# Optimization experiments

Hardware: AMD Instinct MI355X
Metric: run time of the kernel (lower is better)

Reference implementation:

```python
import jax, jax.numpy as jnp
import numpy as np

NB, NA, NDF = 4, 512, 3
N = NB * NA
E_FIX = 40960
RADIUS = 3.1
BOX = 13.9  # box side -> ~20 neighbors within radius 3.1
SQRT3 = float(np.sqrt(3.0))
INV_SQRT2 = float(1.0 / np.sqrt(2.0))
INV_SQRT3 = float(1.0 / np.sqrt(3.0))
INV_SQRT6 = float(1.0 / np.sqrt(6.0))
# e3nn FullyConnectedTensorProduct path weights: sqrt(ir_out.dim / sum_fan_in)
PW1_000 = float(np.sqrt(0.5)); PW1_110 = float(np.sqrt(0.5))
PW1_011 = float(np.sqrt(1.5)); PW1_101 = float(np.sqrt(1.5))
PW1_111 = float(np.sqrt(3.0)); PW1_112 = float(np.sqrt(5.0))
PW2 = float(np.sqrt(3.0 / 128.0))  # fan_in = 64+24+24+16

def _w3j_112():
    # real Wigner-3j (1,1,2), unit Frobenius norm (unique up to sign)
    C = np.zeros((3, 3, 5))
    C[0, 1, 0] = C[1, 0, 0] = 1.0                      # xy
    C[1, 2, 1] = C[2, 1, 1] = 1.0                      # yz
    s = 1.0 / np.sqrt(3.0)
    C[2, 2, 2] = 2 * s; C[0, 0, 2] = -s; C[1, 1, 2] = -s  # 3z^2-r^2
    C[0, 2, 3] = C[2, 0, 3] = 1.0                      # zx
    C[0, 0, 4] = 1.0; C[1, 1, 4] = -1.0                # x^2-y^2
    return (C / np.linalg.norm(C)).astype(np.float32)

C112 = jnp.asarray(_w3j_112())
C211 = jnp.transpose(C112, (2, 0, 1))  # (5,3,3)

def _sh(v):
    # o3.spherical_harmonics(l<=1, normalize=False, 'component'): [1, sqrt(3)*v]
    return jnp.concatenate([jnp.ones(v.shape[:-1] + (1,), v.dtype), SQRT3 * v], axis=-1)

def setup_inputs() -> dict:
    rng = np.random.default_rng(0)
    pos = (rng.random((NB, NA, 3)) * BOX).astype(np.float32)
    srcs, dsts = [], []
    for b in range(NB):  # radius_graph per batch (setup-time, numpy)
        d = np.linalg.norm(pos[b][:, None] - pos[b][None, :], axis=-1)
        m = (d < RADIUS) & ~np.eye(NA, dtype=bool)
        i, j = np.nonzero(m)
        srcs.append(i + b * NA); dsts.append(j + b * NA)
    src = np.concatenate(srcs).astype(np.int64)
    dst = np.concatenate(dsts).astype(np.int64)
    if len(src) >= E_FIX:
        src, dst = src[:E_FIX], dst[:E_FIX]
    else:
        pad = E_FIX - len(src)
        src = np.concatenate([src, np.zeros(pad, np.int64)])
        dst = np.concatenate([dst, np.full(pad, N, np.int64)])  # dummy segment, dropped
    key = jax.random.key(0)
    ks = jax.random.split(key, 12)
    f32 = jnp.float32
    return {
        'node_features': jax.random.randint(ks[0], (NB, NA, NDF), 0, 100),
        'r': jnp.asarray(pos),
        'edge_src': jnp.asarray(src, jnp.int32),
        'edge_dst': jnp.asarray(dst, jnp.int32),
        'emb': jax.random.normal(ks[1], (100, 3), f32),
        't1_000': jax.random.normal(ks[2], (64,), f32),
        't1_011': jax.random.normal(ks[3], (24,), f32),
        't1_101': jax.random.normal(ks[4], (24,), f32),
        't1_110': jax.random.normal(ks[5], (64,), f32),
        't1_111': jax.random.normal(ks[6], (24,), f32),
        't1_112': jax.random.normal(ks[7], (16,), f32),
        't2_0e': jax.random.normal(ks[8], (64,), f32),
        't2_1e': jax.random.normal(ks[9], (24,), f32),
        't2_1o': jax.random.normal(ks[10], (24,), f32),
        't2_2e': jax.random.normal(ks[11], (16,), f32),
    }

def reference(node_features, r, edge_src, edge_dst, emb,
              t1_000, t1_011, t1_101, t1_110, t1_111, t1_112,
              t2_0e, t2_1e, t2_1o, t2_2e):
    nb, na, _ = r.shape
    n = nb * na
    rv = r.reshape(-1, 3)
    evec = rv[edge_src] - rv[edge_dst]
    esh = _sh(evec)                      # [E,4]
    s0, s1 = esh[:, :1], esh[:, 1:]      # [E,1], [E,3]
    nf = node_features.reshape(-1, node_features.shape[-1])
    nfe_sh = _sh(emb[nf])                # [n,NDF,4]

    def seg(x):
        return jax.ops.segment_sum(x, edge_dst, num_segments=n + 1)[:n] * INV_SQRT2

    h = jnp.concatenate([seg(esh)[:, None, :], nfe_sh], axis=1)  # [n,C,4]
    x1 = h[edge_src]                                             # [E,C,4]
    a0, a1 = x1[:, :, 0], x1[:, :, 1:4]
    E_, C_ = a0.shape
    # --- tp1: FullyConnectedTensorProduct(sh, sh -> 64x0e+24x1e+24x1o+16x2e+16x2o)
    o0e = (PW1_000 * (a0 * s0))[..., None] * t1_000 \
        + (PW1_110 * INV_SQRT3) * jnp.einsum('eci,ei->ec', a1, s1)[..., None] * t1_110  # [E,C,64]
    p011 = (PW1_011 * INV_SQRT3) * a0[..., None] * s1[:, None, :]   # [E,C,3]
    p101 = (PW1_101 * INV_SQRT3) * a1 * s0[:, None, :]              # [E,C,3]
    o1o = p011[:, :, None, :] * t1_011[:, None] + p101[:, :, None, :] * t1_101[:, None]  # [E,C,24,3]
    o1e = (PW1_111 * INV_SQRT6) * jnp.cross(a1, s1[:, None, :])[:, :, None, :] * t1_111[:, None]
    o2e = PW1_112 * jnp.einsum('eci,ej,ijk->eck', a1, s1, C112)[:, :, None, :] * t1_112[:, None]
    edge_mid = jnp.concatenate([
        o0e,
        o1o.reshape(E_, C_, 72),
        o1e.reshape(E_, C_, 72),
        o2e.reshape(E_, C_, 80),
        jnp.zeros((E_, C_, 80), x1.dtype),  # 16x2o: no allowed path
    ], axis=-1)                              # [E,C,368]
    h2 = seg(edge_mid)[edge_src]             # [E,C,368]
    # --- tp2: FullyConnectedTensorProduct(mid, sh -> 1x1o)
    m0 = h2[:, :, :64]
    m1e = h2[:, :, 64:136].reshape(E_, C_, 24, 3)
    m1o = h2[:, :, 136:208].reshape(E_, C_, 24, 3)
    m2e = h2[:, :, 208:288].reshape(E_, C_, 16, 5)
    q1 = INV_SQRT3 * jnp.einsum('ecu,ej,u->ecj', m0, s1, t2_0e)
    q2 = INV_SQRT6 * jnp.einsum('ecuk,u->eck', jnp.cross(m1e, s1[:, None, None, :]), t2_1e)
    q3 = INV_SQRT3 * jnp.einsum('ecuj,u->ecj', m1o, t2_1o) * s0[:, None, :]
    q4 = jnp.einsum('ecui,ej,ijk,u->eck', m2e, s1, C211, t2_2e)
    edge_out = PW2 * (q1 + q2 + q3 + q4)     # [E,C,3]
    return seg(edge_out).sum(axis=1).reshape(nb, na, 3)
```

## Files before the change

### kernel.cpp

```cpp
#include <hip/hip_runtime.h>

#define INV_SQRT2 0.70710678118654752f
#define SQRT3     1.73205080756887729f
#define INV_SQRT3 0.57735026918962576f
#define INV_SQRT6 0.40824829046386302f
#define PW1_000   0.70710678118654752f
#define PW1_112   2.23606797749978970f
#define K_P       0.70710678118654752f
#define K_V0      0.40824829046386302f
#define PW2       0.15309310892394863f
#define NC        0.31622776601683794f
#define NC2       0.18257418583505537f

#define RED8(v)  { v += __shfl_xor(v,1,8);  v += __shfl_xor(v,2,8);  v += __shfl_xor(v,4,8); }
#define RED16(v) { v += __shfl_xor(v,1,16); v += __shfl_xor(v,2,16); \
                   v += __shfl_xor(v,4,16); v += __shfl_xor(v,8,16); }

__device__ __forceinline__ int lbound(const int* __restrict__ esrc,
                                      const int* __restrict__ edst,
                                      int n, int E, int target) {
    int lo = 0, hi = E;
    while (lo < hi) {
        int mid = (lo + hi) >> 1;
        int d = edst[mid];
        int key = (d >= n) ? n : esrc[mid];
        if (key < target) lo = mid + 1; else hi = mid;
    }
    return lo;
}

__global__ void __launch_bounds__(256) k_prep(
    const int* __restrict__ nf, const float* __restrict__ rv,
    const int* __restrict__ esrc, const int* __restrict__ edst,
    const float* __restrict__ emb,
    const float* __restrict__ t1_000, const float* __restrict__ t1_011,
    const float* __restrict__ t1_101, const float* __restrict__ t1_110,
    const float* __restrict__ t1_111, const float* __restrict__ t1_112,
    const float* __restrict__ t2_0e, const float* __restrict__ t2_1e,
    const float* __restrict__ t2_1o, const float* __restrict__ t2_2e,
    float* __restrict__ Dd, float4* __restrict__ Hsum,
    int* __restrict__ offs, float4* __restrict__ s1arr,
    int n, int E, int nodeBlocks)
{
    if ((int)blockIdx.x == nodeBlocks) {
        int l = threadIdx.x;
        if (l >= 64) return;
        auto wdot = [&](const float* a, const float* b, int len) -> float {
            float v = (l < len) ? a[l] * b[l] : 0.0f;
            for (int off = 32; off > 0; off >>= 1) v += __shfl_down(v, off);
            return v;
        };
        float d0 = wdot(t1_000, t2_0e, 64);
        float d1 = wdot(t1_110, t2_0e, 64);
        float d2 = wdot(t1_011, t2_1e, 24);
        float d3 = wdot(t1_101, t2_1e, 24);
        float d4 = wdot(t1_111, t2_1o, 24);
        float d5 = wdot(t1_112, t2_2e, 16);
        if (l == 0) { Dd[0]=d0; Dd[1]=d1; Dd[2]=d2; Dd[3]=d3; Dd[4]=d4; Dd[5]=d5; }
        return;
    }
    const int tid = blockIdx.x * 256 + threadIdx.x;
    const int nth = nodeBlocks * 256;

    for (int e = tid; e < E; e += nth) {
        int d = edst[e];
        if (d < n) {
            int s = esrc[e];
            s1arr[e] = make_float4(SQRT3*(rv[d*3+0]-rv[s*3+0]),
                                   SQRT3*(rv[d*3+1]-rv[s*3+1]),
                                   SQRT3*(rv[d*3+2]-rv[s*3+2]),
                                   __int_as_float(d));
        } else {
            s1arr[e] = make_float4(0.f, 0.f, 0.f, __int_as_float(0));
        }
    }

    if (tid < n * 8) {
        int v = tid >> 3, ln = tid & 7;
        int b = 0;
        if (ln == 0) b = lbound(esrc, edst, n, E, v);
        if (ln == 1) b = lbound(esrc, edst, n, E, v + 1);
        int lo = __shfl(b, 0, 8);
        int hi = __shfl(b, 1, 8);
        float sx = 0.f, sy = 0.f, sz = 0.f;
        for (int p = lo + ln; p < hi; p += 8) {
            int j = edst[p];
            sx += rv[j*3+0]; sy += rv[j*3+1]; sz += rv[j*3+2];
        }
        RED8(sx) RED8(sy) RED8(sz)
        if (ln == 0) {
            float cnt = (float)(hi - lo);
            float rx = rv[v*3+0], ry = rv[v*3+1], rz = rv[v*3+2];
            float hx = INV_SQRT2 * SQRT3 * (sx - cnt*rx);
            float hy = INV_SQRT2 * SQRT3 * (sy - cnt*ry);
            float hz = INV_SQRT2 * SQRT3 * (sz - cnt*rz);
            int i0 = nf[v*3+0], i1 = nf[v*3+1], i2 = nf[v*3+2];
            float ex = emb[i0*3+0] + emb[i1*3+0] + emb[i2*3+0];
            float ey = emb[i0*3+1] + emb[i1*3+1] + emb[i2*3+1];
            float ez = emb[i0*3+2] + emb[i1*3+2] + emb[i2*3+2];
            Hsum[v] = make_float4(INV_SQRT2*cnt + 3.0f,
                                  hx + SQRT3*ex, hy + SQRT3*ey, hz + SQRT3*ez);
            offs[v] = lo;
            if (v == n - 1) offs[n] = hi;
        }
    }
}

__global__ void __launch_bounds__(256) k_g2(
    const float4* __restrict__ s1arr, const int* __restrict__ offs,
    const float4* __restrict__ Hsum, float* __restrict__ Mid, int n)
{
    int tid = blockIdx.x * blockDim.x + threadIdx.x;
    if (tid >= n * 16) return;
    int v = tid >> 4, ln = tid & 15;
    int lo = offs[v], hi = offs[v+1];
    float A0=0.f, A1=0.f;
    float px=0.f, py=0.f, pz=0.f;
    float qx=0.f, qy=0.f, qz=0.f;
    float cx=0.f, cy=0.f, cz=0.f;
    float t0=0.f, t1=0.f, t2=0.f, t3=0.f, t4=0.f;
    for (int p = lo + ln; p < hi; p += 16) {
        float4 t = s1arr[p];
        int j = __float_as_int(t.w);
        float s1x = t.x, s1y = t.y, s1z = t.z;
        float4 a = Hsum[j];
        float a0 = a.x, a1x = a.y, a1y = a.z, a1z = a.w;
        A0 += a0;
        A1 += a1x*s1x + a1y*s1y + a1z*s1z;
        px += a0*s1x; py += a0*s1y; pz += a0*s1z;
        qx += a1x;    qy += a1y;    qz += a1z;
        cx += a1y*s1z - a1z*s1y;
        cy += a1z*s1x - a1x*s1z;
        cz += a1x*s1y - a1y*s1x;
        t0 += a1x*s1y + a1y*s1x;
        t1 += a1y*s1z + a1z*s1y;
        t2 += 2.0f*a1z*s1z - a1x*s1x - a1y*s1y;
        t3 += a1x*s1z + a1z*s1x;
        t4 += a1x*s1x - a1y*s1y;
    }
    RED16(A0) RED16(A1)
    RED16(px) RED16(py) RED16(pz)
    RED16(qx) RED16(qy) RED16(qz)
    RED16(cx) RED16(cy) RED16(cz)
    RED16(t0) RED16(t1) RED16(t2) RED16(t3) RED16(t4)
    if (ln == 0) {
        const float kA = INV_SQRT2 * PW1_000;
        const float kB = INV_SQRT2 * K_V0;
        const float kP = INV_SQRT2 * K_P;
        const float kT = INV_SQRT2 * PW1_112 * NC;
        const float kU = INV_SQRT2 * PW1_112 * NC2;
        float4* md = (float4*)(Mid + v*16);
        md[0] = make_float4(kA*A0, kB*A1, kP*px, kP*py);
        md[1] = make_float4(kP*pz, kP*qx, kP*qy, kP*qz);
        md[2] = make_float4(kP*cx, kP*cy, kP*cz, kT*t0);
        md[3] = make_float4(kT*t1, kU*t2, kT*t3, kT*t4);
    }
}

__global__ void __launch_bounds__(256) k_g3(
    const float4* __restrict__ s1arr, const int* __restrict__ offs,
    const float* __restrict__ Mid, const float* __restrict__ Dd,
    float* __restrict__ out, int n)
{
    int tid = blockIdx.x * blockDim.x + threadIdx.x;
    if (tid >= n * 16) return;
    int v = tid >> 4, ln = tid & 15;
    int lo = offs[v], hi = offs[v+1];
    float D00 = Dd[0], D01 = Dd[1], D2a = Dd[2], D2b = Dd[3], D3 = Dd[4], D4 = Dd[5];
    float ox = 0.f, oy = 0.f, oz = 0.f;
    for (int p = lo + ln; p < hi; p += 16) {
        float4 t = s1arr[p];
        int j = __float_as_int(t.w);
        float s1x = t.x, s1y = t.y, s1z = t.z;
        const float4* m4 = (const float4*)(Mid + j*16);
        float4 ga = m4[0], gb = m4[1], gc = m4[2], gd = m4[3];
        float G0=ga.x, G1=ga.y, G2=ga.z, G3=ga.w;
        float G4=gb.x, G5=gb.y, G6=gb.z, G7=gb.w;
        float G8=gc.x, G9=gc.y, G10=gc.z, G11=gc.w;
        float G12=gd.x, G13=gd.y, G14=gd.z, G15=gd.w;
        float q = INV_SQRT3 * (G0*D00 + G1*D01);
        ox += q * s1x; oy += q * s1y; oz += q * s1z;
        float c1x = G3*s1z - G4*s1y;
        float c1y = G4*s1x - G2*s1z;
        float c1z = G2*s1y - G3*s1x;
        float c2x = G6*s1z - G7*s1y;
        float c2y = G7*s1x - G5*s1z;
        float c2z = G5*s1y - G6*s1x;
        ox += INV_SQRT6 * (D2a*c1x + D2b*c2x);
        oy += INV_SQRT6 * (D2a*c1y + D2b*c2y);
        oz += INV_SQRT6 * (D2a*c1z + D2b*c2z);
        ox += INV_SQRT3 * D3 * G8;
        oy += INV_SQRT3 * D3 * G9;
        oz += INV_SQRT3 * D3 * G10;
        ox += D4 * (NC*(s1y*G11 + s1z*G14 + s1x*G15) - NC2*s1x*G13);
        oy += D4 * (NC*(s1x*G11 + s1z*G12 - s1y*G15) - NC2*s1y*G13);
        oz += D4 * (NC*(s1y*G12 + s1x*G14) + 2.0f*NC2*s1z*G13);
    }
    RED16(ox) RED16(oy) RED16(oz)
    if (ln == 0) {
        out[v*3+0] = PW2 * INV_SQRT2 * ox;
        out[v*3+1] = PW2 * INV_SQRT2 * oy;
        out[v*3+2] = PW2 * INV_SQRT2 * oz;
    }
}

extern "C" void kernel_launch(void* const* d_in, const int* in_sizes, int n_in,
                              void* d_out, int out_size, void* d_ws, size_t ws_size,
                              hipStream_t stream) {
    const int*   nf     = (const int*)  d_in[0];
    const float* rv     = (const float*)d_in[1];
    const int*   esrc   = (const int*)  d_in[2];
    const int*   edst   = (const int*)  d_in[3];
    const float* emb    = (const float*)d_in[4];
    const float* t1_000 = (const float*)d_in[5];
    const float* t1_011 = (const float*)d_in[6];
    const float* t1_101 = (const float*)d_in[7];
    const float* t1_110 = (const float*)d_in[8];
    const float* t1_111 = (const float*)d_in[9];
    const float* t1_112 = (const float*)d_in[10];
    const float* t2_0e  = (const float*)d_in[11];
    const float* t2_1e  = (const float*)d_in[12];
    const float* t2_1o  = (const float*)d_in[13];
    const float* t2_2e  = (const float*)d_in[14];

    const int n = in_sizes[1] / 3;
    const int E = in_sizes[2];

    float4* Hsum  = (float4*)d_ws;
    float4* s1arr = Hsum + n;
    float*  Mid   = (float*)(s1arr + E);
    float*  Dd    = Mid + (size_t)n * 16;
    int*    offs  = (int*)(Dd + 8);
    float*  out   = (float*)d_out;

    const int nodeBlocks = (n * 8 + 255) / 256;
    k_prep<<<nodeBlocks + 1, 256, 0, stream>>>(
        nf, rv, esrc, edst, emb,
        t1_000, t1_011, t1_101, t1_110, t1_111, t1_112,
        t2_0e, t2_1e, t2_1o, t2_2e,
        Dd, Hsum, offs, s1arr, n, E, nodeBlocks);
    k_g2<<<(n * 16 + 255) / 256, 256, 0, stream>>>(s1arr, offs, Hsum, Mid, n);
    k_g3<<<(n * 16 + 255) / 256, 256, 0, stream>>>(s1arr, offs, Mid, Dd, out, n);
}
```

Baseline: 21.74 us.

## Fuse the two gather kernels by recomputing neighbor intermediates inline

The separate per-edge s1 precompute and the node-level Mid kernel are removed. The output kernel now recomputes each neighbor's 16-value intermediate inline by walking that neighbor's own edge list. A 64-lane wavefront per node splits neighbors across 16 slots with 4 lanes per sub-loop. This removes one kernel launch and the workspace round trips for s1arr and Mid. The cost is redundant recomputation, roughly degree-squared gathers per node.

```diff
diff --git a/kernel.cpp b/kernel.cpp
--- a/kernel.cpp
+++ b/kernel.cpp
@@ -13,8 +13,6 @@
 #define NC2       0.18257418583505537f
 
 #define RED8(v)  { v += __shfl_xor(v,1,8);  v += __shfl_xor(v,2,8);  v += __shfl_xor(v,4,8); }
-#define RED16(v) { v += __shfl_xor(v,1,16); v += __shfl_xor(v,2,16); \
-                   v += __shfl_xor(v,4,16); v += __shfl_xor(v,8,16); }
 
 __device__ __forceinline__ int lbound(const int* __restrict__ esrc,
                                       const int* __restrict__ edst,
@@ -39,8 +37,7 @@
     const float* __restrict__ t2_0e, const float* __restrict__ t2_1e,
     const float* __restrict__ t2_1o, const float* __restrict__ t2_2e,
     float* __restrict__ Dd, float4* __restrict__ Hsum,
-    int* __restrict__ offs, float4* __restrict__ s1arr,
-    int n, int E, int nodeBlocks)
+    int* __restrict__ offs, int n, int E, int nodeBlocks)
 {
     if ((int)blockIdx.x == nodeBlocks) {
         int l = threadIdx.x;
@@ -60,126 +57,91 @@
         return;
     }
     const int tid = blockIdx.x * 256 + threadIdx.x;
-    const int nth = nodeBlocks * 256;
-
-    for (int e = tid; e < E; e += nth) {
-        int d = edst[e];
-        if (d < n) {
-            int s = esrc[e];
-            s1arr[e] = make_float4(SQRT3*(rv[d*3+0]-rv[s*3+0]),
-                                   SQRT3*(rv[d*3+1]-rv[s*3+1]),
-                                   SQRT3*(rv[d*3+2]-rv[s*3+2]),
-                                   __int_as_float(d));
-        } else {
-            s1arr[e] = make_float4(0.f, 0.f, 0.f, __int_as_float(0));
+    if (tid >= n * 8) return;
+    int v = tid >> 3, ln = tid & 7;
+    int b = 0;
+    if (ln == 0) b = lbound(esrc, edst, n, E, v);
+    if (ln == 1) b = lbound(esrc, edst, n, E, v + 1);
+    int lo = __shfl(b, 0, 8);
+    int hi = __shfl(b, 1, 8);
+    float sx = 0.f, sy = 0.f, sz = 0.f;
+    for (int p = lo + ln; p < hi; p += 8) {
+        int j = edst[p];
+        sx += rv[j*3+0]; sy += rv[j*3+1]; sz += rv[j*3+2];
+    }
+    RED8(sx) RED8(sy) RED8(sz)
+    if (ln == 0) {
+        float cnt = (float)(hi - lo);
+        float rx = rv[v*3+0], ry = rv[v*3+1], rz = rv[v*3+2];
+        int i0 = nf[v*3+0], i1 = nf[v*3+1], i2 = nf[v*3+2];
+        float ex = emb[i0*3+0] + emb[i1*3+0] + emb[i2*3+0];
+        float ey = emb[i0*3+1] + emb[i1*3+1] + emb[i2*3+1];
+        float ez = emb[i0*3+2] + emb[i1*3+2] + emb[i2*3+2];
+        Hsum[v] = make_float4(INV_SQRT2*cnt + 3.0f,
+                              INV_SQRT2*SQRT3*(sx - cnt*rx) + SQRT3*ex,
+                              INV_SQRT2*SQRT3*(sy - cnt*ry) + SQRT3*ey,
+                              INV_SQRT2*SQRT3*(sz - cnt*rz) + SQRT3*ez);
+        offs[v] = lo;
+        if (v == n - 1) offs[n] = hi;
+    }
+}
+
+__global__ void __launch_bounds__(256) k_out(
+    const float* __restrict__ rv, const int* __restrict__ edst,
+    const float4* __restrict__ Hsum, const int* __restrict__ offs,
+    const float* __restrict__ Dd, float* __restrict__ out, int n)
+{
+    const int gid = blockIdx.x * 256 + threadIdx.x;
+    const int v = gid >> 6, ln = gid & 63;
+    if (v >= n) return;
+    const int lo = offs[v], hi = offs[v+1];
+    const float rvx = rv[v*3+0], rvy = rv[v*3+1], rvz = rv[v*3+2];
+    const float D00 = Dd[0], D01 = Dd[1], D2a = Dd[2], D2b = Dd[3], D3 = Dd[4], D4 = Dd[5];
+    const float kA = INV_SQRT2 * PW1_000;
+    const float kB = INV_SQRT2 * K_V0;
+    const float kP = INV_SQRT2 * K_P;
+    const float kT = INV_SQRT2 * PW1_112 * NC;
+    const float kU = INV_SQRT2 * PW1_112 * NC2;
+    const int jslot = ln >> 2, ksub = ln & 3;
+    float ox = 0.f, oy = 0.f, oz = 0.f;
+
+    for (int p = lo + jslot; p < hi; p += 16) {
+        int j = edst[p];
+        float rjx = rv[j*3+0], rjy = rv[j*3+1], rjz = rv[j*3+2];
+        float s1x = SQRT3*(rjx - rvx), s1y = SQRT3*(rjy - rvy), s1z = SQRT3*(rjz - rvz);
+        int qlo = offs[j], qhi = offs[j+1];
+        float A0=0.f, A1=0.f;
+        float px=0.f, py=0.f, pz=0.f;
+        float qx=0.f, qy=0.f, qz=0.f;
+        float cx=0.f, cy=0.f, cz=0.f;
+        float u0=0.f, u1=0.f, u2=0.f, u3=0.f, u4=0.f;
+        for (int q = qlo + ksub; q < qhi; q += 4) {
+            int k = edst[q];
+            float w1x = SQRT3*(rv[k*3+0] - rjx);
+            float w1y = SQRT3*(rv[k*3+1] - rjy);
+            float w1z = SQRT3*(rv[k*3+2] - rjz);
+            float4 a = Hsum[k];
+            float a0 = a.x, a1x = a.y, a1y = a.z, a1z = a.w;
+            A0 += a0;
+            A1 += a1x*w1x + a1y*w1y + a1z*w1z;
+            px += a0*w1x; py += a0*w1y; pz += a0*w1z;
+            qx += a1x;    qy += a1y;    qz += a1z;
+            cx += a1y*w1z - a1z*w1y;
+            cy += a1z*w1x - a1x*w1z;
+            cz += a1x*w1y - a1y*w1x;
+            u0 += a1x*w1y + a1y*w1x;
+            u1 += a1y*w1z + a1z*w1y;
+            u2 += 2.0f*a1z*w1z - a1x*w1x - a1y*w1y;
+            u3 += a1x*w1z + a1z*w1x;
+            u4 += a1x*w1x - a1y*w1y;
         }
-    }
-
-    if (tid < n * 8) {
-        int v = tid >> 3, ln = tid & 7;
-        int b = 0;
-        if (ln == 0) b = lbound(esrc, edst, n, E, v);
-        if (ln == 1) b = lbound(esrc, edst, n, E, v + 1);
-        int lo = __shfl(b, 0, 8);
-        int hi = __shfl(b, 1, 8);
-        float sx = 0.f, sy = 0.f, sz = 0.f;
-        for (int p = lo + ln; p < hi; p += 8) {
-            int j = edst[p];
-            sx += rv[j*3+0]; sy += rv[j*3+1]; sz += rv[j*3+2];
-        }
-        RED8(sx) RED8(sy) RED8(sz)
-        if (ln == 0) {
-            float cnt = (float)(hi - lo);
-            float rx = rv[v*3+0], ry = rv[v*3+1], rz = rv[v*3+2];
-            float hx = INV_SQRT2 * SQRT3 * (sx - cnt*rx);
-            float hy = INV_SQRT2 * SQRT3 * (sy - cnt*ry);
-            float hz = INV_SQRT2 * SQRT3 * (sz - cnt*rz);
-            int i0 = nf[v*3+0], i1 = nf[v*3+1], i2 = nf[v*3+2];
-            float ex = emb[i0*3+0] + emb[i1*3+0] + emb[i2*3+0];
-            float ey = emb[i0*3+1] + emb[i1*3+1] + emb[i2*3+1];
-            float ez = emb[i0*3+2] + emb[i1*3+2] + emb[i2*3+2];
-            Hsum[v] = make_float4(INV_SQRT2*cnt + 3.0f,
-                                  hx + SQRT3*ex, hy + SQRT3*ey, hz + SQRT3*ez);
-            offs[v] = lo;
-            if (v == n - 1) offs[n] = hi;
-        }
-    }
-}
-
-__global__ void __launch_bounds__(256) k_g2(
-    const float4* __restrict__ s1arr, const int* __restrict__ offs,
-    const float4* __restrict__ Hsum, float* __restrict__ Mid, int n)
-{
-    int tid = blockIdx.x * blockDim.x + threadIdx.x;
-    if (tid >= n * 16) return;
-    int v = tid >> 4, ln = tid & 15;
-    int lo = offs[v], hi = offs[v+1];
-    float A0=0.f, A1=0.f;
-    float px=0.f, py=0.f, pz=0.f;
-    float qx=0.f, qy=0.f, qz=0.f;
-    float cx=0.f, cy=0.f, cz=0.f;
-    float t0=0.f, t1=0.f, t2=0.f, t3=0.f, t4=0.f;
-    for (int p = lo + ln; p < hi; p += 16) {
-        float4 t = s1arr[p];
-        int j = __float_as_int(t.w);
-        float s1x = t.x, s1y = t.y, s1z = t.z;
-        float4 a = Hsum[j];
-        float a0 = a.x, a1x = a.y, a1y = a.z, a1z = a.w;
-        A0 += a0;
-        A1 += a1x*s1x + a1y*s1y + a1z*s1z;
-        px += a0*s1x; py += a0*s1y; pz += a0*s1z;
-        qx += a1x;    qy += a1y;    qz += a1z;
-        cx += a1y*s1z - a1z*s1y;
-        cy += a1z*s1x - a1x*s1z;
-        cz += a1x*s1y - a1y*s1x;
-        t0 += a1x*s1y + a1y*s1x;
-        t1 += a1y*s1z + a1z*s1y;
-        t2 += 2.0f*a1z*s1z - a1x*s1x - a1y*s1y;
-        t3 += a1x*s1z + a1z*s1x;
-        t4 += a1x*s1x - a1y*s1y;
-    }
-    RED16(A0) RED16(A1)
-    RED16(px) RED16(py) RED16(pz)
-    RED16(qx) RED16(qy) RED16(qz)
-    RED16(cx) RED16(cy) RED16(cz)
-    RED16(t0) RED16(t1) RED16(t2) RED16(t3) RED16(t4)
-    if (ln == 0) {
-        const float kA = INV_SQRT2 * PW1_000;
-        const float kB = INV_SQRT2 * K_V0;
-        const float kP = INV_SQRT2 * K_P;
-        const float kT = INV_SQRT2 * PW1_112 * NC;
-        const float kU = INV_SQRT2 * PW1_112 * NC2;
-        float4* md = (float4*)(Mid + v*16);
-        md[0] = make_float4(kA*A0, kB*A1, kP*px, kP*py);
-        md[1] = make_float4(kP*pz, kP*qx, kP*qy, kP*qz);
-        md[2] = make_float4(kP*cx, kP*cy, kP*cz, kT*t0);
-        md[3] = make_float4(kT*t1, kU*t2, kT*t3, kT*t4);
-    }
-}
-
-__global__ void __launch_bounds__(256) k_g3(
-    const float4* __restrict__ s1arr, const int* __restrict__ offs,
-    const float* __restrict__ Mid, const float* __restrict__ Dd,
-    float* __restrict__ out, int n)
-{
-    int tid = blockIdx.x * blockDim.x + threadIdx.x;
-    if (tid >= n * 16) return;
-    int v = tid >> 4, ln = tid & 15;
-    int lo = offs[v], hi = offs[v+1];
-    float D00 = Dd[0], D01 = Dd[1], D2a = Dd[2], D2b = Dd[3], D3 = Dd[4], D4 = Dd[5];
-    float ox = 0.f, oy = 0.f, oz = 0.f;
-    for (int p = lo + ln; p < hi; p += 16) {
-        float4 t = s1arr[p];
-        int j = __float_as_int(t.w);
-        float s1x = t.x, s1y = t.y, s1z = t.z;
-        const float4* m4 = (const float4*)(Mid + j*16);
-        float4 ga = m4[0], gb = m4[1], gc = m4[2], gd = m4[3];
-        float G0=ga.x, G1=ga.y, G2=ga.z, G3=ga.w;
-        float G4=gb.x, G5=gb.y, G6=gb.z, G7=gb.w;
-        float G8=gc.x, G9=gc.y, G10=gc.z, G11=gc.w;
-        float G12=gd.x, G13=gd.y, G14=gd.z, G15=gd.w;
-        float q = INV_SQRT3 * (G0*D00 + G1*D01);
-        ox += q * s1x; oy += q * s1y; oz += q * s1z;
+        float G0 = kA*A0, G1 = kB*A1;
+        float G2 = kP*px, G3 = kP*py, G4 = kP*pz;
+        float G5 = kP*qx, G6 = kP*qy, G7 = kP*qz;
+        float G8 = kP*cx, G9 = kP*cy, G10 = kP*cz;
+        float G11 = kT*u0, G12 = kT*u1, G13 = kU*u2, G14 = kT*u3, G15 = kT*u4;
+        float q1 = INV_SQRT3 * (G0*D00 + G1*D01);
+        ox += q1 * s1x; oy += q1 * s1y; oz += q1 * s1z;
         float c1x = G3*s1z - G4*s1y;
         float c1y = G4*s1x - G2*s1z;
         float c1z = G2*s1y - G3*s1x;
@@ -196,7 +158,11 @@
         oy += D4 * (NC*(s1x*G11 + s1z*G12 - s1y*G15) - NC2*s1y*G13);
         oz += D4 * (NC*(s1y*G12 + s1x*G14) + 2.0f*NC2*s1z*G13);
     }
-    RED16(ox) RED16(oy) RED16(oz)
+    for (int m = 1; m < 64; m <<= 1) {
+        ox += __shfl_xor(ox, m);
+        oy += __shfl_xor(oy, m);
+        oz += __shfl_xor(oz, m);
+    }
     if (ln == 0) {
         out[v*3+0] = PW2 * INV_SQRT2 * ox;
         out[v*3+1] = PW2 * INV_SQRT2 * oy;
@@ -226,19 +192,17 @@
     const int n = in_sizes[1] / 3;
     const int E = in_sizes[2];
 
-    float4* Hsum  = (float4*)d_ws;
-    float4* s1arr = Hsum + n;
-    float*  Mid   = (float*)(s1arr + E);
-    float*  Dd    = Mid + (size_t)n * 16;
-    int*    offs  = (int*)(Dd + 8);
-    float*  out   = (float*)d_out;
+    float4* Hsum = (float4*)d_ws;
+    float*  Dd   = (float*)(Hsum + n);
+    int*    offs = (int*)(Dd + 8);
+    float*  out  = (float*)d_out;
 
     const int nodeBlocks = (n * 8 + 255) / 256;
     k_prep<<<nodeBlocks + 1, 256, 0, stream>>>(
         nf, rv, esrc, edst, emb,
         t1_000, t1_011, t1_101, t1_110, t1_111, t1_112,
         t2_0e, t2_1e, t2_1o, t2_2e,
-        Dd, Hsum, offs, s1arr, n, E, nodeBlocks);
-    k_g2<<<(n * 16 + 255) / 256, 256, 0, stream>>>(s1arr, offs, Hsum, Mid, n);
-    k_g3<<<(n * 16 + 255) / 256, 256, 0, stream>>>(s1arr, offs, Mid, Dd, out, n);
-}
+        Dd, Hsum, offs, n, E, nodeBlocks);
+    k_out<<<(n * 64 + 255) / 256, 256, 0, stream>>>(
+        rv, edst, Hsum, offs, Dd, out, n);
+}
```

Result: slower. 26.02 us (+19.7%).

## Drop precomputed edge-vector array and speed up CSR offset search with shared samples

Applied to the files above, without the earlier changes.

Removes the per-edge s1arr float4 buffer written in k_prep; k_g2 and k_g3 now recompute the edge vector from edst and rv on the fly, saving a 40960-entry write and two reads of it. The global binary search for CSR offsets is replaced by a two-level search: each block loads a 1281-entry sampled key table into shared memory, then does a short global search within one stride. This trades the per-edge buffer for extra gather loads of rv in the two edge kernels, and every block now pays for sampling the table.

```diff
diff --git a/kernel.cpp b/kernel.cpp
--- a/kernel.cpp
+++ b/kernel.cpp
@@ -16,18 +16,7 @@
 #define RED16(v) { v += __shfl_xor(v,1,16); v += __shfl_xor(v,2,16); \
                    v += __shfl_xor(v,4,16); v += __shfl_xor(v,8,16); }
 
-__device__ __forceinline__ int lbound(const int* __restrict__ esrc,
-                                      const int* __restrict__ edst,
-                                      int n, int E, int target) {
-    int lo = 0, hi = E;
-    while (lo < hi) {
-        int mid = (lo + hi) >> 1;
-        int d = edst[mid];
-        int key = (d >= n) ? n : esrc[mid];
-        if (key < target) lo = mid + 1; else hi = mid;
-    }
-    return lo;
-}
+#define NS 1280
 
 __global__ void __launch_bounds__(256) k_prep(
     const int* __restrict__ nf, const float* __restrict__ rv,
@@ -39,8 +28,7 @@
     const float* __restrict__ t2_0e, const float* __restrict__ t2_1e,
     const float* __restrict__ t2_1o, const float* __restrict__ t2_2e,
     float* __restrict__ Dd, float4* __restrict__ Hsum,
-    int* __restrict__ offs, float4* __restrict__ s1arr,
-    int n, int E, int nodeBlocks)
+    int* __restrict__ offs, int n, int E, int nodeBlocks)
 {
     if ((int)blockIdx.x == nodeBlocks) {
         int l = threadIdx.x;
@@ -59,70 +47,80 @@
         if (l == 0) { Dd[0]=d0; Dd[1]=d1; Dd[2]=d2; Dd[3]=d3; Dd[4]=d4; Dd[5]=d5; }
         return;
     }
+
+    __shared__ int ks[NS + 1];
+    const int ST = (E + NS - 1) / NS;
+    for (int i = threadIdx.x; i <= NS; i += 256) {
+        int p = i * ST;
+        int key;
+        if (p >= E) key = n;
+        else { int d = edst[p]; key = (d >= n) ? n : esrc[p]; }
+        ks[i] = key;
+    }
+    __syncthreads();
+
     const int tid = blockIdx.x * 256 + threadIdx.x;
-    const int nth = nodeBlocks * 256;
-
-    for (int e = tid; e < E; e += nth) {
-        int d = edst[e];
-        if (d < n) {
-            int s = esrc[e];
-            s1arr[e] = make_float4(SQRT3*(rv[d*3+0]-rv[s*3+0]),
-                                   SQRT3*(rv[d*3+1]-rv[s*3+1]),
-                                   SQRT3*(rv[d*3+2]-rv[s*3+2]),
-                                   __int_as_float(d));
-        } else {
-            s1arr[e] = make_float4(0.f, 0.f, 0.f, __int_as_float(0));
+    if (tid >= n * 8) return;
+    int v = tid >> 3, ln = tid & 7;
+    int b = 0;
+    if (ln < 2) {
+        int target = v + ln;
+        int lo = 0, hi = NS + 1;
+        while (lo < hi) { int m = (lo + hi) >> 1; if (ks[m] < target) lo = m + 1; else hi = m; }
+        int glo = (lo == 0) ? 0 : (lo - 1) * ST;
+        int ghi = lo * ST; if (ghi > E) ghi = E;
+        while (glo < ghi) {
+            int m = (glo + ghi) >> 1;
+            int d = edst[m];
+            int k = (d >= n) ? n : esrc[m];
+            if (k < target) glo = m + 1; else ghi = m;
         }
-    }
-
-    if (tid < n * 8) {
-        int v = tid >> 3, ln = tid & 7;
-        int b = 0;
-        if (ln == 0) b = lbound(esrc, edst, n, E, v);
-        if (ln == 1) b = lbound(esrc, edst, n, E, v + 1);
-        int lo = __shfl(b, 0, 8);
-        int hi = __shfl(b, 1, 8);
-        float sx = 0.f, sy = 0.f, sz = 0.f;
-        for (int p = lo + ln; p < hi; p += 8) {
-            int j = edst[p];
-            sx += rv[j*3+0]; sy += rv[j*3+1]; sz += rv[j*3+2];
-        }
-        RED8(sx) RED8(sy) RED8(sz)
-        if (ln == 0) {
-            float cnt = (float)(hi - lo);
-            float rx = rv[v*3+0], ry = rv[v*3+1], rz = rv[v*3+2];
-            float hx = INV_SQRT2 * SQRT3 * (sx - cnt*rx);
-            float hy = INV_SQRT2 * SQRT3 * (sy - cnt*ry);
-            float hz = INV_SQRT2 * SQRT3 * (sz - cnt*rz);
-            int i0 = nf[v*3+0], i1 = nf[v*3+1], i2 = nf[v*3+2];
-            float ex = emb[i0*3+0] + emb[i1*3+0] + emb[i2*3+0];
-            float ey = emb[i0*3+1] + emb[i1*3+1] + emb[i2*3+1];
-            float ez = emb[i0*3+2] + emb[i1*3+2] + emb[i2*3+2];
-            Hsum[v] = make_float4(INV_SQRT2*cnt + 3.0f,
-                                  hx + SQRT3*ex, hy + SQRT3*ey, hz + SQRT3*ez);
-            offs[v] = lo;
-            if (v == n - 1) offs[n] = hi;
-        }
+        b = glo;
+    }
+    int lo = __shfl(b, 0, 8);
+    int hi = __shfl(b, 1, 8);
+    float sx = 0.f, sy = 0.f, sz = 0.f;
+    for (int p = lo + ln; p < hi; p += 8) {
+        int j = edst[p];
+        sx += rv[j*3+0]; sy += rv[j*3+1]; sz += rv[j*3+2];
+    }
+    RED8(sx) RED8(sy) RED8(sz)
+    if (ln == 0) {
+        float cnt = (float)(hi - lo);
+        float rx = rv[v*3+0], ry = rv[v*3+1], rz = rv[v*3+2];
+        int i0 = nf[v*3+0], i1 = nf[v*3+1], i2 = nf[v*3+2];
+        float ex = emb[i0*3+0] + emb[i1*3+0] + emb[i2*3+0];
+        float ey = emb[i0*3+1] + emb[i1*3+1] + emb[i2*3+1];
+        float ez = emb[i0*3+2] + emb[i1*3+2] + emb[i2*3+2];
+        Hsum[v] = make_float4(INV_SQRT2*cnt + 3.0f,
+                              INV_SQRT2*SQRT3*(sx - cnt*rx) + SQRT3*ex,
+                              INV_SQRT2*SQRT3*(sy - cnt*ry) + SQRT3*ey,
+                              INV_SQRT2*SQRT3*(sz - cnt*rz) + SQRT3*ez);
+        offs[v] = lo;
+        if (v == n - 1) offs[n] = hi;
     }
 }
 
 __global__ void __launch_bounds__(256) k_g2(
-    const float4* __restrict__ s1arr, const int* __restrict__ offs,
-    const float4* __restrict__ Hsum, float* __restrict__ Mid, int n)
+    const float* __restrict__ rv, const int* __restrict__ edst,
+    const int* __restrict__ offs, const float4* __restrict__ Hsum,
+    float* __restrict__ Mid, int n)
 {
     int tid = blockIdx.x * blockDim.x + threadIdx.x;
     if (tid >= n * 16) return;
     int v = tid >> 4, ln = tid & 15;
     int lo = offs[v], hi = offs[v+1];
+    float rvx = rv[v*3+0], rvy = rv[v*3+1], rvz = rv[v*3+2];
     float A0=0.f, A1=0.f;
     float px=0.f, py=0.f, pz=0.f;
     float qx=0.f, qy=0.f, qz=0.f;
     float cx=0.f, cy=0.f, cz=0.f;
     float t0=0.f, t1=0.f, t2=0.f, t3=0.f, t4=0.f;
     for (int p = lo + ln; p < hi; p += 16) {
-        float4 t = s1arr[p];
-        int j = __float_as_int(t.w);
-        float s1x = t.x, s1y = t.y, s1z = t.z;
+        int j = edst[p];
+        float s1x = SQRT3*(rv[j*3+0] - rvx);
+        float s1y = SQRT3*(rv[j*3+1] - rvy);
+        float s1z = SQRT3*(rv[j*3+2] - rvz);
         float4 a = Hsum[j];
         float a0 = a.x, a1x = a.y, a1y = a.z, a1z = a.w;
         A0 += a0;
@@ -158,20 +156,22 @@
 }
 
 __global__ void __launch_bounds__(256) k_g3(
-    const float4* __restrict__ s1arr, const int* __restrict__ offs,
-    const float* __restrict__ Mid, const float* __restrict__ Dd,
-    float* __restrict__ out, int n)
+    const float* __restrict__ rv, const int* __restrict__ edst,
+    const int* __restrict__ offs, const float* __restrict__ Mid,
+    const float* __restrict__ Dd, float* __restrict__ out, int n)
 {
     int tid = blockIdx.x * blockDim.x + threadIdx.x;
     if (tid >= n * 16) return;
     int v = tid >> 4, ln = tid & 15;
     int lo = offs[v], hi = offs[v+1];
+    float rvx = rv[v*3+0], rvy = rv[v*3+1], rvz = rv[v*3+2];
     float D00 = Dd[0], D01 = Dd[1], D2a = Dd[2], D2b = Dd[3], D3 = Dd[4], D4 = Dd[5];
     float ox = 0.f, oy = 0.f, oz = 0.f;
     for (int p = lo + ln; p < hi; p += 16) {
-        float4 t = s1arr[p];
-        int j = __float_as_int(t.w);
-        float s1x = t.x, s1y = t.y, s1z = t.z;
+        int j = edst[p];
+        float s1x = SQRT3*(rv[j*3+0] - rvx);
+        float s1y = SQRT3*(rv[j*3+1] - rvy);
+        float s1z = SQRT3*(rv[j*3+2] - rvz);
         const float4* m4 = (const float4*)(Mid + j*16);
         float4 ga = m4[0], gb = m4[1], gc = m4[2], gd = m4[3];
         float G0=ga.x, G1=ga.y, G2=ga.z, G3=ga.w;
@@ -226,19 +226,18 @@
     const int n = in_sizes[1] / 3;
     const int E = in_sizes[2];
 
-    float4* Hsum  = (float4*)d_ws;
-    float4* s1arr = Hsum + n;
-    float*  Mid   = (float*)(s1arr + E);
-    float*  Dd    = Mid + (size_t)n * 16;
-    int*    offs  = (int*)(Dd + 8);
-    float*  out   = (float*)d_out;
+    float4* Hsum = (float4*)d_ws;
+    float*  Mid  = (float*)(Hsum + n);
+    float*  Dd   = Mid + (size_t)n * 16;
+    int*    offs = (int*)(Dd + 8);
+    float*  out  = (float*)d_out;
 
     const int nodeBlocks = (n * 8 + 255) / 256;
     k_prep<<<nodeBlocks + 1, 256, 0, stream>>>(
         nf, rv, esrc, edst, emb,
         t1_000, t1_011, t1_101, t1_110, t1_111, t1_112,
         t2_0e, t2_1e, t2_1o, t2_2e,
-        Dd, Hsum, offs, s1arr, n, E, nodeBlocks);
-    k_g2<<<(n * 16 + 255) / 256, 256, 0, stream>>>(s1arr, offs, Hsum, Mid, n);
-    k_g3<<<(n * 16 + 255) / 256, 256, 0, stream>>>(s1arr, offs, Mid, Dd, out, n);
-}
+        Dd, Hsum, offs, n, E, nodeBlocks);
+    k_g2<<<(n * 16 + 255) / 256, 256, 0, stream>>>(rv, edst, offs, Hsum, Mid, n);
+    k_g3<<<(n * 16 + 255) / 256, 256, 0, stream>>>(rv, edst, offs, Mid, Dd, out, n);
+}
```

After: 18.12 us. -16.7%, faster.
